# Performance work log

Measured on AMD Instinct MI355X. Metric: run time of the kernel, lower is better.

## Reference

```python
import jax, jax.numpy as jnp
import numpy as np

N_WIRES = 16
N_LAYERS = 6
BATCH = 128


def setup_inputs() -> dict:
    key = jax.random.key(0)
    k1, k2 = jax.random.split(key)
    # embedding angles in [-pi, pi]
    x = jax.random.uniform(k1, (BATCH, N_WIRES), jnp.float32, -np.pi, np.pi)
    # StronglyEntanglingLayers weights, as in __init__: 0.2 * normal
    w = 0.2 * jax.random.normal(k2, (N_LAYERS, N_WIRES, 3), jnp.float32)
    return {"x": x, "w": w}


def _apply_1q(psi, U, wire, n):
    # psi: (B, 2^n) complex; U: (2,2) or (B,2,2) complex. Wire 0 = most significant bit.
    B = psi.shape[0]
    psi = psi.reshape(B, 2 ** wire, 2, -1)
    if U.ndim == 2:
        out = jnp.einsum('ab,nlbr->nlar', U, psi)
    else:
        out = jnp.einsum('nab,nlbr->nlar', U, psi)
    return out.reshape(B, -1)


def _apply_cnot(psi, c, t, n):
    # CNOT with control c, target t: flip target axis on the control=1 subspace.
    B = psi.shape[0]
    psi = psi.reshape((B,) + (2,) * n)
    ac, at = c + 1, t + 1  # tensor axes (axis 0 is batch)
    a0 = jnp.take(psi, 0, axis=ac)
    a1 = jnp.take(psi, 1, axis=ac)
    t_ax = at - 1 if at > ac else at  # target axis after removing control axis
    a1 = jnp.flip(a1, axis=t_ax)
    psi = jnp.stack([a0, a1], axis=ac)
    return psi.reshape(B, -1)


def _rot_matrix(phi, theta, omega):
    # PennyLane Rot(phi, theta, omega) = RZ(omega) RY(theta) RZ(phi)
    c, s = jnp.cos(theta / 2), jnp.sin(theta / 2)
    m00 = jnp.exp(-0.5j * (phi + omega)) * c
    m01 = -jnp.exp(0.5j * (phi - omega)) * s
    m10 = jnp.exp(-0.5j * (phi - omega)) * s
    m11 = jnp.exp(0.5j * (phi + omega)) * c
    return jnp.stack([jnp.stack([m00, m01]), jnp.stack([m10, m11])]).astype(jnp.complex64)


def _circuit(x, w):
    B, n = x.shape
    n_layers = w.shape[0]
    psi = jnp.zeros((B, 2 ** n), jnp.complex64).at[:, 0].set(1.0)

    # AngleEmbedding, rotation='Y': RY(x_i) on wire i (batched 2x2, real entries)
    c, s = jnp.cos(x / 2), jnp.sin(x / 2)  # (B, n)
    for i in range(n):
        U = jnp.stack([jnp.stack([c[:, i], -s[:, i]], -1),
                       jnp.stack([s[:, i], c[:, i]], -1)], -2).astype(jnp.complex64)
        psi = _apply_1q(psi, U, i, n)

    # StronglyEntanglingLayers: per layer, Rot on every wire then ring of CNOTs
    for l in range(n_layers):
        for i in range(n):
            U = _rot_matrix(w[l, i, 0], w[l, i, 1], w[l, i, 2])
            psi = _apply_1q(psi, U, i, n)
        r = (l % (n - 1)) + 1 if n > 1 else 0  # default PennyLane ranges
        if r:
            for i in range(n):
                psi = _apply_cnot(psi, i, (i + r) % n, n)

    # <Z_i> = P(bit_i = 0) - P(bit_i = 1)
    probs = psi.real ** 2 + psi.imag ** 2  # (B, 2^n)
    p = probs.reshape((B,) + (2,) * n)
    z = []
    for i in range(n):
        axes = tuple(a for a in range(1, n + 1) if a != i + 1)
        m = p.sum(axis=axes)  # (B, 2)
        z.append(m[:, 0] - m[:, 1])
    return jnp.stack(z, axis=-1).astype(jnp.float32)  # (B, n_wires)


def reference(x, w):
    return _circuit(x, w)
```

## Files before the change

### kernel.cpp

```cpp
#include <hip/hip_runtime.h>
#include <utility>


#define NW    16
#define BLK   1024
#define CHUNK 16384

template<class F, int... Is>
__device__ __forceinline__ void static_for_impl(F&& f, std::integer_sequence<int, Is...>) {
    (f(std::integral_constant<int, Is>{}), ...);
}
template<int N, class F>
__device__ __forceinline__ void static_for(F&& f) {
    static_for_impl(f, std::make_integer_sequence<int, N>{});
}

__device__ __forceinline__ int swz(int u) { return u ^ (((u >> 4) & 7) << 1); }

__device__ __forceinline__ void c2x2(float2& a0, float2& a1,
                                     float2 m00, float2 m01,
                                     float2 m10, float2 m11) {
    float2 r0, r1;
    r0.x = m00.x*a0.x - m00.y*a0.y + m01.x*a1.x - m01.y*a1.y;
    r0.y = m00.x*a0.y + m00.y*a0.x + m01.x*a1.y + m01.y*a1.x;
    r1.x = m10.x*a0.x - m10.y*a0.y + m11.x*a1.x - m11.y*a1.y;
    r1.y = m10.x*a0.y + m10.y*a0.x + m11.x*a1.y + m11.y*a1.x;
    a0 = r0; a1 = r1;
}

__device__ __forceinline__ float2 cmul(float2 a, float2 b) {
    return make_float2(a.x*b.x - a.y*b.y, a.x*b.y + a.y*b.x);
}

template<int Q>
__device__ __forceinline__ void rot_regs(float2 a[16], float2 m00, float2 m01,
                                         float2 m10, float2 m11) {
#pragma unroll
    for (int j = 0; j < 16; ++j)
        if (!((j >> Q) & 1))
            c2x2(a[j], a[j | (1 << Q)], m00, m01, m10, m11);
}

template<int QC, int QT>
__device__ __forceinline__ void cnot_inreg(float2 a[16]) {
#pragma unroll
    for (int j = 0; j < 16; ++j)
        if (((j >> QC) & 1) && !((j >> QT) & 1)) {
            float2 t = a[j]; a[j] = a[j | (1 << QT)]; a[j | (1 << QT)] = t;
        }
}

template<int QT>
__device__ __forceinline__ void cnot_ctrlout(float2 a[16], int ctrl) {
#pragma unroll
    for (int j = 0; j < 16; ++j)
        if (!((j >> QT) & 1)) {
            int j2 = j | (1 << QT);
            float2 x = a[j], y = a[j2];
            a[j].x  = ctrl ? y.x : x.x;  a[j].y  = ctrl ? y.y : x.y;
            a[j2].x = ctrl ? x.x : y.x;  a[j2].y = ctrl ? x.y : y.y;
        }
}

__device__ __forceinline__ void rot_mat(const float* ww, float2 m[4]) {
    float phi = ww[0], th = ww[1], om = ww[2];
    float ct, st;   sincosf(0.5f * th, &st, &ct);
    float cap, sap; sincosf(0.5f * (phi + om), &sap, &cap);
    float cam, sam; sincosf(0.5f * (phi - om), &sam, &cam);
    m[0] = make_float2( cap * ct, -sap * ct);
    m[1] = make_float2(-cam * st, -sam * st);
    m[2] = make_float2( cam * st, -sam * st);
    m[3] = make_float2( cap * ct,  sap * ct);
}

template<int L, int S>
__device__ __forceinline__ int sweep_gates(float2 a[16], const float2 (*gm)[4],
                                           int ub, int c14) {
    constexpr int r    = L + 1;
    constexpr int base = (S == 1) ? 10 : (S == 2) ? 6 : (S == 3) ? 2 : 0;
    constexpr int plo  = base;
    constexpr int phi  = (S == 4) ? 1 : base + 3;
    int wmask = 0;
    static_for<phi - plo + 1>([&](auto K) {
        constexpr int bb = phi - decltype(K)::value;
        if constexpr (bb != 15 - r && !(L == 0 && bb == 14 - r)) {
            constexpr int wire = 15 - bb;
            rot_regs<bb - base>(a, gm[wire][0], gm[wire][1], gm[wire][2], gm[wire][3]);
        }
    });
    if constexpr (L >= 1 && (14 - r) >= plo && (14 - r) <= phi)
        cnot_ctrlout<14 - r - base>(a, c14);
    static_for<14 - r>([&](auto K) {
        constexpr int i  = 2 + decltype(K)::value;
        constexpr int cb = 15 - i, tb = cb - r;
        if constexpr (tb >= plo && tb <= phi) {
            if constexpr (cb <= base + 3) {
                cnot_inreg<cb - base, tb - base>(a);
            } else if constexpr (tb - r >= plo) {
                cnot_ctrlout<tb - base>(a, (ub >> cb) & 1);
            } else {
                wmask |= ((ub >> cb) & 1) << (tb - base);
            }
        }
    });
    return wmask;
}

template<int L>
__global__ __launch_bounds__(BLK)
void k_p1(const float* __restrict__ w, float2* __restrict__ psi) {
    constexpr int r  = L + 1;
    constexpr int G1 = 14 - L;
    const int b = blockIdx.x >> 2, m = blockIdx.x & 3;
    const int T = (m << 10) | (int)threadIdx.x;
    float2* g = psi + ((size_t)b << 16);

    const int sb = ((T & ((1 << (13 - L)) - 1)) << 1) | ((T >> (13 - L)) << (15 - L));

    float2 m0[4], m1[4], mr[4];
    rot_mat(w + (L * NW + 0) * 3, m0);
    rot_mat(w + (L * NW + 1) * 3, m1);
    rot_mat(w + (L * NW + r) * 3, mr);

    float2 a[16];
#pragma unroll
    for (int jh = 0; jh < 8; ++jh) {
        int s = sb | ((jh & 1) << G1) | (((jh >> 1) & 1) << 14) | (((jh >> 2) & 1) << 15);
        float4 f = *reinterpret_cast<const float4*>(g + s);
        a[(jh << 1)]     = make_float2(f.x, f.y);
        a[(jh << 1) | 1] = make_float2(f.z, f.w);
    }

    if constexpr (L == 1) {
        cnot_inreg<0, 3>(a);
    } else if constexpr (L == 2) {
        cnot_ctrlout<3>(a, (sb >> 1) & 1);
        cnot_inreg<0, 2>(a);
    } else {
        cnot_ctrlout<3>(a, (sb >> (L - 1)) & 1);
        cnot_ctrlout<2>(a, (sb >> (L - 2)) & 1);
    }
    rot_regs<3>(a, m0[0], m0[1], m0[2], m0[3]);
    rot_regs<2>(a, m1[0], m1[1], m1[2], m1[3]);
    rot_regs<1>(a, mr[0], mr[1], mr[2], mr[3]);
    cnot_inreg<3, 1>(a);

#pragma unroll
    for (int jh = 0; jh < 8; ++jh) {
        int s = sb | ((jh & 1) << G1) | (((jh >> 1) & 1) << 14) | (((jh >> 2) & 1) << 15);
        float2 lo = a[(jh << 1)], hi = a[(jh << 1) | 1];
        *reinterpret_cast<float4*>(g + s) = make_float4(lo.x, lo.y, hi.x, hi.y);
    }
}

template<int L>
__global__ __launch_bounds__(BLK)
void k_p2(const float* __restrict__ x, const float* __restrict__ w,
          float* __restrict__ out, float2* __restrict__ psi) {
    constexpr int r = L + 1;
    __shared__ float2 lds[CHUNK];
    __shared__ float2 gm[NW][4];
    __shared__ float  ecs[NW], ess[NW], accs[NW];
    const int b = blockIdx.x >> 2, c = blockIdx.x & 3;
    const int tid = threadIdx.x;
    const int c14 = c & 1;
    float2* g = psi + ((size_t)b << 16) + ((size_t)c << 14);

    if (tid < NW) {
        rot_mat(w + (L * NW + tid) * 3, gm[tid]);
        if (L == 0) {
            float s_, c_; sincosf(0.5f * x[b * NW + tid], &s_, &c_);
            ecs[tid] = c_; ess[tid] = s_;
        }
        if (L == 5) accs[tid] = 0.f;
    }

    if constexpr (L >= 1) {
#pragma unroll
        for (int it = 0; it < 8; ++it) {
            int v = tid + it * BLK;
            float4 f = reinterpret_cast<const float4*>(g)[v];
            int u = swz(2 * v);
            lds[u]     = make_float2(f.x, f.y);
            lds[u ^ 1] = make_float2(f.z, f.w);
        }
    }
    __syncthreads();

    float2 a[16];
    {
        const int ub = tid;
        if constexpr (L == 0) {
            float2 v[3][2];
#pragma unroll
            for (int wq = 0; wq < 3; ++wq)
#pragma unroll
                for (int bb = 0; bb < 2; ++bb) {
                    v[wq][bb].x = gm[wq][2*bb].x * ecs[wq] + gm[wq][2*bb+1].x * ess[wq];
                    v[wq][bb].y = gm[wq][2*bb].y * ecs[wq] + gm[wq][2*bb+1].y * ess[wq];
                }
            const int b0 = (c >> 1) & 1, b1 = c & 1;
            float2 psiC[2];
#pragma unroll
            for (int b2 = 0; b2 < 2; ++b2)
                psiC[b2] = cmul(cmul(v[0][b0], v[1][b1 ^ b0]), v[2][b2 ^ b1]);
            float plo = 1.0f;
#pragma unroll
            for (int k = 0; k < 10; ++k)
                plo *= ((tid >> k) & 1) ? ess[15 - k] : ecs[15 - k];
#pragma unroll
            for (int j = 0; j < 16; ++j) {
                float f3 = ((j >> 2) & 1) ? ess[3] : ecs[3];
                float f4 = ((j >> 1) & 1) ? ess[4] : ecs[4];
                float f5 = (j & 1)        ? ess[5] : ecs[5];
                float hb = f3 * f4 * f5 * plo;
                float2 pc = psiC[(j >> 3) & 1];
                a[j] = make_float2(pc.x * hb, pc.y * hb);
            }
        } else {
#pragma unroll
            for (int j = 0; j < 16; ++j) a[j] = lds[swz(ub | (j << 10))];
        }
        int wm = sweep_gates<L, 1>(a, gm, ub, c14) << 10;
#pragma unroll
        for (int j = 0; j < 16; ++j) lds[swz((ub | (j << 10)) ^ wm)] = a[j];
    }
    __syncthreads();
    {
        const int ub = (tid & 63) | ((tid >> 6) << 10);
#pragma unroll
        for (int j = 0; j < 16; ++j) a[j] = lds[swz(ub | (j << 6))];
        int wm = sweep_gates<L, 2>(a, gm, ub, c14) << 6;
#pragma unroll
        for (int j = 0; j < 16; ++j) lds[swz((ub | (j << 6)) ^ wm)] = a[j];
    }
    __syncthreads();
    {
        const int ub = (tid & 3) | ((tid >> 2) << 6);
#pragma unroll
        for (int j = 0; j < 16; ++j) a[j] = lds[swz(ub | (j << 2))];
        int wm = sweep_gates<L, 3>(a, gm, ub, c14) << 2;
#pragma unroll
        for (int j = 0; j < 16; ++j) lds[swz((ub | (j << 2)) ^ wm)] = a[j];
    }
    __syncthreads();
    {
        const int ub = tid << 4;
#pragma unroll
        for (int j = 0; j < 16; ++j) a[j] = lds[swz(ub | j)];
        int wm = sweep_gates<L, 4>(a, gm, ub, c14);
#pragma unroll
        for (int j = 0; j < 16; ++j) lds[swz((ub | j) ^ wm)] = a[j];
    }
    __syncthreads();

    if constexpr (L == 5) {
        const int ub = tid;
        float psum = 0.f, z2s = 0.f, z3s = 0.f, z4s = 0.f, z5s = 0.f;
#pragma unroll
        for (int j = 0; j < 16; ++j) {
            float2 v2 = lds[swz(ub | (j << 10))];
            float p = v2.x * v2.x + v2.y * v2.y;
            psum += p;
            z2s += (j & 8) ? -p : p;
            z3s += (j & 4) ? -p : p;
            z4s += (j & 2) ? -p : p;
            z5s += (j & 1) ? -p : p;
        }
        float z[NW];
        z[0] = (((c >> 1) ^ (tid >> 5)) & 1) ? -psum : psum;
        z[1] = (((c) ^ (tid >> 4)) & 1) ? -psum : psum;
        z[2] = ((tid >> 3) & 1) ? -z2s : z2s;
        z[3] = ((tid >> 2) & 1) ? -z3s : z3s;
        z[4] = ((tid >> 1) & 1) ? -z4s : z4s;
        z[5] = (tid & 1) ? -z5s : z5s;
#pragma unroll
        for (int i = 6; i < NW; ++i)
            z[i] = ((tid >> (15 - i)) & 1) ? -psum : psum;
#pragma unroll
        for (int i = 0; i < NW; ++i) {
            float v2 = z[i];
#pragma unroll
            for (int off = 32; off > 0; off >>= 1) v2 += __shfl_down(v2, off, 64);
            if ((tid & 63) == 0) atomicAdd(&accs[i], v2);
        }
        __syncthreads();
        if (tid < NW) atomicAdd(&out[b * NW + tid], accs[tid]);
    } else {
#pragma unroll
        for (int it = 0; it < 8; ++it) {
            int v = tid + it * BLK;
            int u = 2 * v;
            int wm0 = 0, wm1 = 0;
            static_for<(r >= 3) ? (r - 2) : 0>([&](auto K) {
                constexpr int k  = decltype(K)::value;
                constexpr int cb = r - 3 - k, tb = 13 - k;
                wm0 |= ((u >> cb) & 1) << tb;
                wm1 |= (((u | 1) >> cb) & 1) << tb;
            });
            float2 lo = lds[swz(u ^ wm0)];
            float2 hi = lds[swz((u | 1) ^ wm1)];
            reinterpret_cast<float4*>(g)[v] = make_float4(lo.x, lo.y, hi.x, hi.y);
        }
    }
}

extern "C" void kernel_launch(void* const* d_in, const int* in_sizes, int n_in,
                              void* d_out, int out_size, void* d_ws, size_t ws_size,
                              hipStream_t stream) {
    const float* x = (const float*)d_in[0];
    const float* w = (const float*)d_in[1];
    float* out = (float*)d_out;
    float2* psi = (float2*)d_ws;

    const int batch = in_sizes[0] / NW;
    const int grid  = batch * 4;

    hipMemsetAsync(d_out, 0, (size_t)out_size * sizeof(float), stream);

    k_p2<0><<<grid, BLK, 0, stream>>>(x, w, out, psi);
    k_p1<1><<<grid, BLK, 0, stream>>>(w, psi);
    k_p2<1><<<grid, BLK, 0, stream>>>(x, w, out, psi);
    k_p1<2><<<grid, BLK, 0, stream>>>(w, psi);
    k_p2<2><<<grid, BLK, 0, stream>>>(x, w, out, psi);
    k_p1<3><<<grid, BLK, 0, stream>>>(w, psi);
    k_p2<3><<<grid, BLK, 0, stream>>>(x, w, out, psi);
    k_p1<4><<<grid, BLK, 0, stream>>>(w, psi);
    k_p2<4><<<grid, BLK, 0, stream>>>(x, w, out, psi);
    k_p1<5><<<grid, BLK, 0, stream>>>(w, psi);
    k_p2<5><<<grid, BLK, 0, stream>>>(x, w, out, psi);
}
```

Baseline: 573.1 us.

## Split state into 8 chunks per sample with padded LDS and fused gather

Each phase-2 kernel now handles 8K-amplitude chunks with 512 threads instead of 16K with 1024, and repartitions which wires live in the per-block chunk versus the phase-1 kernel. The XOR swizzle is replaced by padding every 16 elements to avoid LDS bank conflicts. The first sweep now loads straight from global memory, skipping the separate LDS staging pass, and the final expectation reduction works from registers without writing back to LDS. The intent is to raise occupancy (launch_bounds 512,4) and cut LDS traffic. The cost is extra gate bookkeeping in phase 1 and more blocks, with a risk of uncoalesced global reads in the first sweep.

```diff
diff --git a/kernel.cpp b/kernel.cpp
--- a/kernel.cpp
+++ b/kernel.cpp
@@ -3,8 +3,10 @@
 
 
 #define NW    16
-#define BLK   1024
-#define CHUNK 16384
+#define P1BLK 1024
+#define P2BLK 512
+#define CHUNK 8192
+#define LDSN  (CHUNK + CHUNK / 16)
 
 template<class F, int... Is>
 __device__ __forceinline__ void static_for_impl(F&& f, std::integer_sequence<int, Is...>) {
@@ -15,7 +17,7 @@
     static_for_impl(f, std::make_integer_sequence<int, N>{});
 }
 
-__device__ __forceinline__ int swz(int u) { return u ^ (((u >> 4) & 7) << 1); }
+__device__ __forceinline__ int pidx(int u) { return u + (u >> 4); }
 
 __device__ __forceinline__ void c2x2(float2& a0, float2& a1,
                                      float2 m00, float2 m01,
@@ -73,98 +75,108 @@
     m[3] = make_float2( cap * ct,  sap * ct);
 }
 
+constexpr int swof(int tb) { return tb >= 9 ? 1 : tb >= 5 ? 2 : tb >= 1 ? 3 : 4; }
+
 template<int L, int S>
 __device__ __forceinline__ int sweep_gates(float2 a[16], const float2 (*gm)[4],
-                                           int ub, int c14) {
+                                           int ub, int c) {
     constexpr int r    = L + 1;
-    constexpr int base = (S == 1) ? 10 : (S == 2) ? 6 : (S == 3) ? 2 : 0;
-    constexpr int plo  = base;
-    constexpr int phi  = (S == 4) ? 1 : base + 3;
+    constexpr int base = (S == 1) ? 9 : (S == 2) ? 5 : (S == 3) ? 1 : 0;
+    constexpr int rlo  = base;
+    constexpr int rhi  = (S == 1) ? 12 : (S == 2) ? 8 : (S == 3) ? 4 : 0;
+    static_for<rhi - rlo + 1>([&](auto K) {
+        constexpr int bb   = rhi - decltype(K)::value;
+        constexpr int wire = 15 - bb;
+        rot_regs<bb - base>(a, gm[wire][0], gm[wire][1], gm[wire][2], gm[wire][3]);
+    });
     int wmask = 0;
-    static_for<phi - plo + 1>([&](auto K) {
-        constexpr int bb = phi - decltype(K)::value;
-        if constexpr (bb != 15 - r && !(L == 0 && bb == 14 - r)) {
-            constexpr int wire = 15 - bb;
-            rot_regs<bb - base>(a, gm[wire][0], gm[wire][1], gm[wire][2], gm[wire][3]);
-        }
-    });
-    if constexpr (L >= 1 && (14 - r) >= plo && (14 - r) <= phi)
-        cnot_ctrlout<14 - r - base>(a, c14);
-    static_for<14 - r>([&](auto K) {
-        constexpr int i  = 2 + decltype(K)::value;
-        constexpr int cb = 15 - i, tb = cb - r;
-        if constexpr (tb >= plo && tb <= phi) {
-            if constexpr (cb <= base + 3) {
-                cnot_inreg<cb - base, tb - base>(a);
-            } else if constexpr (tb - r >= plo) {
-                cnot_ctrlout<tb - base>(a, (ub >> cb) & 1);
-            } else {
-                wmask |= ((ub >> cb) & 1) << (tb - base);
+    static_for<16>([&](auto I) {
+        constexpr int i = decltype(I)::value;
+        if constexpr (i + r < 16) {
+            constexpr int cb = 15 - i, tb = cb - r;
+            constexpr bool skip = (L == 0 && i <= 1) || (L == 1 && i == 0);
+            if constexpr (!skip && swof(tb) == S) {
+                if constexpr (cb >= base && cb <= base + 3) {
+                    cnot_inreg<cb - base, tb - base>(a);
+                } else {
+                    int ctrl = (cb >= 13) ? ((c >> (cb - 13)) & 1)
+                                          : ((ub >> cb) & 1);
+                    constexpr int ts = tb - r;
+                    if constexpr (ts >= 0 && swof(ts) == S)
+                        cnot_ctrlout<tb - base>(a, ctrl);
+                    else
+                        wmask |= ctrl << (tb - base);
+                }
             }
         }
     });
     return wmask;
 }
 
-template<int L>
-__global__ __launch_bounds__(BLK)
+template<int LL>
+__global__ __launch_bounds__(P1BLK)
 void k_p1(const float* __restrict__ w, float2* __restrict__ psi) {
-    constexpr int r  = L + 1;
-    constexpr int G1 = 14 - L;
-    const int b = blockIdx.x >> 2, m = blockIdx.x & 3;
-    const int T = (m << 10) | (int)threadIdx.x;
+    const int b = blockIdx.x >> 2;
+    const int T = ((blockIdx.x & 3) << 10) | (int)threadIdx.x;
     float2* g = psi + ((size_t)b << 16);
-
-    const int sb = ((T & ((1 << (13 - L)) - 1)) << 1) | ((T >> (13 - L)) << (15 - L));
-
-    float2 m0[4], m1[4], mr[4];
-    rot_mat(w + (L * NW + 0) * 3, m0);
-    rot_mat(w + (L * NW + 1) * 3, m1);
-    rot_mat(w + (L * NW + r) * 3, mr);
+    const int sb = T << 1;
+
+    float2 m0[4], m1[4], m2[4];
+    rot_mat(w + (LL * NW + 0) * 3, m0);
+    rot_mat(w + (LL * NW + 1) * 3, m1);
+    rot_mat(w + (LL * NW + 2) * 3, m2);
 
     float2 a[16];
 #pragma unroll
     for (int jh = 0; jh < 8; ++jh) {
-        int s = sb | ((jh & 1) << G1) | (((jh >> 1) & 1) << 14) | (((jh >> 2) & 1) << 15);
+        int s = sb | ((jh & 1) << 13) | (((jh >> 1) & 1) << 14) | (((jh >> 2) & 1) << 15);
         float4 f = *reinterpret_cast<const float4*>(g + s);
         a[(jh << 1)]     = make_float2(f.x, f.y);
         a[(jh << 1) | 1] = make_float2(f.z, f.w);
     }
 
-    if constexpr (L == 1) {
+    if constexpr (LL == 1) {
         cnot_inreg<0, 3>(a);
-    } else if constexpr (L == 2) {
+    } else if constexpr (LL == 2) {
         cnot_ctrlout<3>(a, (sb >> 1) & 1);
         cnot_inreg<0, 2>(a);
+    } else if constexpr (LL == 3) {
+        cnot_ctrlout<3>(a, (sb >> 2) & 1);
+        cnot_ctrlout<2>(a, (sb >> 1) & 1);
+        cnot_inreg<0, 1>(a);
+    } else if constexpr (LL == 4) {
+        cnot_ctrlout<3>(a, (sb >> 3) & 1);
+        cnot_ctrlout<2>(a, (sb >> 2) & 1);
+        cnot_ctrlout<1>(a, (sb >> 1) & 1);
     } else {
-        cnot_ctrlout<3>(a, (sb >> (L - 1)) & 1);
-        cnot_ctrlout<2>(a, (sb >> (L - 2)) & 1);
-    }
+        cnot_ctrlout<3>(a, (sb >> 4) & 1);
+        cnot_ctrlout<2>(a, (sb >> 3) & 1);
+        cnot_ctrlout<1>(a, (sb >> 2) & 1);
+    }
+
     rot_regs<3>(a, m0[0], m0[1], m0[2], m0[3]);
     rot_regs<2>(a, m1[0], m1[1], m1[2], m1[3]);
-    rot_regs<1>(a, mr[0], mr[1], mr[2], mr[3]);
-    cnot_inreg<3, 1>(a);
+    rot_regs<1>(a, m2[0], m2[1], m2[2], m2[3]);
+    if constexpr (LL == 1) cnot_inreg<3, 1>(a);
 
 #pragma unroll
     for (int jh = 0; jh < 8; ++jh) {
-        int s = sb | ((jh & 1) << G1) | (((jh >> 1) & 1) << 14) | (((jh >> 2) & 1) << 15);
+        int s = sb | ((jh & 1) << 13) | (((jh >> 1) & 1) << 14) | (((jh >> 2) & 1) << 15);
         float2 lo = a[(jh << 1)], hi = a[(jh << 1) | 1];
         *reinterpret_cast<float4*>(g + s) = make_float4(lo.x, lo.y, hi.x, hi.y);
     }
 }
 
 template<int L>
-__global__ __launch_bounds__(BLK)
+__global__ __launch_bounds__(P2BLK, 4)
 void k_p2(const float* __restrict__ x, const float* __restrict__ w,
           float* __restrict__ out, float2* __restrict__ psi) {
-    constexpr int r = L + 1;
-    __shared__ float2 lds[CHUNK];
+    __shared__ float2 lds[LDSN];
     __shared__ float2 gm[NW][4];
     __shared__ float  ecs[NW], ess[NW], accs[NW];
-    const int b = blockIdx.x >> 2, c = blockIdx.x & 3;
+    const int b = blockIdx.x >> 3, c = blockIdx.x & 7;
     const int tid = threadIdx.x;
-    const int c14 = c & 1;
-    float2* g = psi + ((size_t)b << 16) + ((size_t)c << 14);
+    float2* g = psi + ((size_t)b << 16) + ((size_t)c << 13);
 
     if (tid < NW) {
         rot_mat(w + (L * NW + tid) * 3, gm[tid]);
@@ -174,17 +186,6 @@
         }
         if (L == 5) accs[tid] = 0.f;
     }
-
-    if constexpr (L >= 1) {
-#pragma unroll
-        for (int it = 0; it < 8; ++it) {
-            int v = tid + it * BLK;
-            float4 f = reinterpret_cast<const float4*>(g)[v];
-            int u = swz(2 * v);
-            lds[u]     = make_float2(f.x, f.y);
-            lds[u ^ 1] = make_float2(f.z, f.w);
-        }
-    }
     __syncthreads();
 
     float2 a[16];
@@ -199,108 +200,108 @@
                     v[wq][bb].x = gm[wq][2*bb].x * ecs[wq] + gm[wq][2*bb+1].x * ess[wq];
                     v[wq][bb].y = gm[wq][2*bb].y * ecs[wq] + gm[wq][2*bb+1].y * ess[wq];
                 }
-            const int b0 = (c >> 1) & 1, b1 = c & 1;
-            float2 psiC[2];
-#pragma unroll
-            for (int b2 = 0; b2 < 2; ++b2)
-                psiC[b2] = cmul(cmul(v[0][b0], v[1][b1 ^ b0]), v[2][b2 ^ b1]);
+            const int c2 = (c >> 2) & 1, c1 = (c >> 1) & 1, c0 = c & 1;
+            float2 cs = cmul(cmul(v[0][c2], v[1][c1 ^ c2]), v[2][c0 ^ c1]);
             float plo = 1.0f;
 #pragma unroll
-            for (int k = 0; k < 10; ++k)
+            for (int k = 0; k < 9; ++k)
                 plo *= ((tid >> k) & 1) ? ess[15 - k] : ecs[15 - k];
 #pragma unroll
             for (int j = 0; j < 16; ++j) {
-                float f3 = ((j >> 2) & 1) ? ess[3] : ecs[3];
-                float f4 = ((j >> 1) & 1) ? ess[4] : ecs[4];
-                float f5 = (j & 1)        ? ess[5] : ecs[5];
-                float hb = f3 * f4 * f5 * plo;
-                float2 pc = psiC[(j >> 3) & 1];
-                a[j] = make_float2(pc.x * hb, pc.y * hb);
+                float f = plo * ((j & 8) ? ess[3] : ecs[3])
+                              * ((j & 4) ? ess[4] : ecs[4])
+                              * ((j & 2) ? ess[5] : ecs[5])
+                              * ((j & 1) ? ess[6] : ecs[6]);
+                a[j] = make_float2(cs.x * f, cs.y * f);
             }
         } else {
 #pragma unroll
-            for (int j = 0; j < 16; ++j) a[j] = lds[swz(ub | (j << 10))];
-        }
-        int wm = sweep_gates<L, 1>(a, gm, ub, c14) << 10;
-#pragma unroll
-        for (int j = 0; j < 16; ++j) lds[swz((ub | (j << 10)) ^ wm)] = a[j];
+            for (int j = 0; j < 16; ++j)
+                a[j] = g[tid | (j << 9)];
+        }
+        int wm = sweep_gates<L, 1>(a, gm, ub, c) << 9;
+#pragma unroll
+        for (int j = 0; j < 16; ++j) lds[pidx((tid | (j << 9)) ^ wm)] = a[j];
     }
     __syncthreads();
     {
-        const int ub = (tid & 63) | ((tid >> 6) << 10);
-#pragma unroll
-        for (int j = 0; j < 16; ++j) a[j] = lds[swz(ub | (j << 6))];
-        int wm = sweep_gates<L, 2>(a, gm, ub, c14) << 6;
-#pragma unroll
-        for (int j = 0; j < 16; ++j) lds[swz((ub | (j << 6)) ^ wm)] = a[j];
+        const int ub = (tid & 31) | ((tid >> 5) << 9);
+#pragma unroll
+        for (int j = 0; j < 16; ++j) a[j] = lds[pidx(ub | (j << 5))];
+        int wm = sweep_gates<L, 2>(a, gm, ub, c) << 5;
+#pragma unroll
+        for (int j = 0; j < 16; ++j) lds[pidx((ub | (j << 5)) ^ wm)] = a[j];
     }
     __syncthreads();
     {
-        const int ub = (tid & 3) | ((tid >> 2) << 6);
-#pragma unroll
-        for (int j = 0; j < 16; ++j) a[j] = lds[swz(ub | (j << 2))];
-        int wm = sweep_gates<L, 3>(a, gm, ub, c14) << 2;
-#pragma unroll
-        for (int j = 0; j < 16; ++j) lds[swz((ub | (j << 2)) ^ wm)] = a[j];
+        const int ub = (tid & 1) | ((tid >> 1) << 5);
+#pragma unroll
+        for (int j = 0; j < 16; ++j) a[j] = lds[pidx(ub | (j << 1))];
+        int wm = sweep_gates<L, 3>(a, gm, ub, c) << 1;
+#pragma unroll
+        for (int j = 0; j < 16; ++j) lds[pidx((ub | (j << 1)) ^ wm)] = a[j];
     }
     __syncthreads();
     {
         const int ub = tid << 4;
 #pragma unroll
-        for (int j = 0; j < 16; ++j) a[j] = lds[swz(ub | j)];
-        int wm = sweep_gates<L, 4>(a, gm, ub, c14);
-#pragma unroll
-        for (int j = 0; j < 16; ++j) lds[swz((ub | j) ^ wm)] = a[j];
-    }
-    __syncthreads();
-
-    if constexpr (L == 5) {
-        const int ub = tid;
-        float psum = 0.f, z2s = 0.f, z3s = 0.f, z4s = 0.f, z5s = 0.f;
-#pragma unroll
-        for (int j = 0; j < 16; ++j) {
-            float2 v2 = lds[swz(ub | (j << 10))];
-            float p = v2.x * v2.x + v2.y * v2.y;
-            psum += p;
-            z2s += (j & 8) ? -p : p;
-            z3s += (j & 4) ? -p : p;
-            z4s += (j & 2) ? -p : p;
-            z5s += (j & 1) ? -p : p;
-        }
-        float z[NW];
-        z[0] = (((c >> 1) ^ (tid >> 5)) & 1) ? -psum : psum;
-        z[1] = (((c) ^ (tid >> 4)) & 1) ? -psum : psum;
-        z[2] = ((tid >> 3) & 1) ? -z2s : z2s;
-        z[3] = ((tid >> 2) & 1) ? -z3s : z3s;
-        z[4] = ((tid >> 1) & 1) ? -z4s : z4s;
-        z[5] = (tid & 1) ? -z5s : z5s;
-#pragma unroll
-        for (int i = 6; i < NW; ++i)
-            z[i] = ((tid >> (15 - i)) & 1) ? -psum : psum;
-#pragma unroll
-        for (int i = 0; i < NW; ++i) {
-            float v2 = z[i];
-#pragma unroll
-            for (int off = 32; off > 0; off >>= 1) v2 += __shfl_down(v2, off, 64);
-            if ((tid & 63) == 0) atomicAdd(&accs[i], v2);
-        }
-        __syncthreads();
-        if (tid < NW) atomicAdd(&out[b * NW + tid], accs[tid]);
-    } else {
-#pragma unroll
-        for (int it = 0; it < 8; ++it) {
-            int v = tid + it * BLK;
-            int u = 2 * v;
-            int wm0 = 0, wm1 = 0;
-            static_for<(r >= 3) ? (r - 2) : 0>([&](auto K) {
-                constexpr int k  = decltype(K)::value;
-                constexpr int cb = r - 3 - k, tb = 13 - k;
-                wm0 |= ((u >> cb) & 1) << tb;
-                wm1 |= (((u | 1) >> cb) & 1) << tb;
-            });
-            float2 lo = lds[swz(u ^ wm0)];
-            float2 hi = lds[swz((u | 1) ^ wm1)];
-            reinterpret_cast<float4*>(g)[v] = make_float4(lo.x, lo.y, hi.x, hi.y);
+        for (int j = 0; j < 16; ++j) a[j] = lds[pidx(ub | j)];
+        int wm = sweep_gates<L, 4>(a, gm, ub, c);
+
+        if constexpr (L == 5) {
+            float psum = 0.f, sb3 = 0.f, sb2 = 0.f, sb1 = 0.f, sb0 = 0.f;
+#pragma unroll
+            for (int j = 0; j < 16; ++j) {
+                int jj = j ^ wm;
+                float2 v2 = a[j];
+                float p = v2.x * v2.x + v2.y * v2.y;
+                psum += p;
+                sb3 += (jj & 8) ? -p : p;
+                sb2 += (jj & 4) ? -p : p;
+                sb1 += (jj & 2) ? -p : p;
+                sb0 += (jj & 1) ? -p : p;
+            }
+            const int c2 = (c >> 2) & 1, c1 = (c >> 1) & 1, c0 = c & 1;
+            float z[NW];
+            z[0]  = ((c2 ^ (tid >> 1)) & 1) ? -psum : psum;
+            z[1]  = ((c1 ^ tid) & 1)        ? -psum : psum;
+            z[2]  = c0 ? -sb3 : sb3;
+            z[3]  = ((tid >> 8) & 1) ? -sb2 : sb2;
+            z[4]  = ((tid >> 7) & 1) ? -sb1 : sb1;
+            z[5]  = ((tid >> 6) & 1) ? -sb0 : sb0;
+#pragma unroll
+            for (int i = 6; i < 12; ++i)
+                z[i] = ((tid >> (11 - i)) & 1) ? -psum : psum;
+            z[12] = sb3; z[13] = sb2; z[14] = sb1; z[15] = sb0;
+#pragma unroll
+            for (int i = 0; i < NW; ++i) {
+                float v2 = z[i];
+#pragma unroll
+                for (int off = 32; off > 0; off >>= 1)
+                    v2 += __shfl_down(v2, off, 64);
+                if ((tid & 63) == 0) atomicAdd(&accs[i], v2);
+            }
+            __syncthreads();
+            if (tid < NW) atomicAdd(&out[b * NW + tid], accs[tid]);
+        } else {
+#pragma unroll
+            for (int j = 0; j < 16; ++j) lds[pidx((ub | j) ^ wm)] = a[j];
+            __syncthreads();
+#pragma unroll
+            for (int it = 0; it < CHUNK / 2 / P2BLK; ++it) {
+                int v = tid + it * P2BLK;
+                int u = 2 * v;
+                int wm0 = 0, wm1 = 0;
+                static_for<(L >= 3) ? (L - 2) : 0>([&](auto K) {
+                    constexpr int k  = decltype(K)::value;
+                    constexpr int cbb = L - 3 - k, tbb = 12 - k;
+                    wm0 |= ((u >> cbb) & 1) << tbb;
+                    wm1 |= (((u | 1) >> cbb) & 1) << tbb;
+                });
+                float2 lo = lds[pidx(u ^ wm0)];
+                float2 hi = lds[pidx((u | 1) ^ wm1)];
+                reinterpret_cast<float4*>(g)[v] = make_float4(lo.x, lo.y, hi.x, hi.y);
+            }
         }
     }
 }
@@ -314,19 +315,20 @@
     float2* psi = (float2*)d_ws;
 
     const int batch = in_sizes[0] / NW;
-    const int grid  = batch * 4;
+    const int g1 = batch * 4;
+    const int g2 = batch * 8;
 
     hipMemsetAsync(d_out, 0, (size_t)out_size * sizeof(float), stream);
 
-    k_p2<0><<<grid, BLK, 0, stream>>>(x, w, out, psi);
-    k_p1<1><<<grid, BLK, 0, stream>>>(w, psi);
-    k_p2<1><<<grid, BLK, 0, stream>>>(x, w, out, psi);
-    k_p1<2><<<grid, BLK, 0, stream>>>(w, psi);
-    k_p2<2><<<grid, BLK, 0, stream>>>(x, w, out, psi);
-    k_p1<3><<<grid, BLK, 0, stream>>>(w, psi);
-    k_p2<3><<<grid, BLK, 0, stream>>>(x, w, out, psi);
-    k_p1<4><<<grid, BLK, 0, stream>>>(w, psi);
-    k_p2<4><<<grid, BLK, 0, stream>>>(x, w, out, psi);
-    k_p1<5><<<grid, BLK, 0, stream>>>(w, psi);
-    k_p2<5><<<grid, BLK, 0, stream>>>(x, w, out, psi);
-}
+    k_p2<0><<<g2, P2BLK, 0, stream>>>(x, w, out, psi);
+    k_p1<1><<<g1, P1BLK, 0, stream>>>(w, psi);
+    k_p2<1><<<g2, P2BLK, 0, stream>>>(x, w, out, psi);
+    k_p1<2><<<g1, P1BLK, 0, stream>>>(w, psi);
+    k_p2<2><<<g2, P2BLK, 0, stream>>>(x, w, out, psi);
+    k_p1<3><<<g1, P1BLK, 0, stream>>>(w, psi);
+    k_p2<3><<<g2, P2BLK, 0, stream>>>(x, w, out, psi);
+    k_p1<4><<<g1, P1BLK, 0, stream>>>(w, psi);
+    k_p2<4><<<g2, P2BLK, 0, stream>>>(x, w, out, psi);
+    k_p1<5><<<g1, P1BLK, 0, stream>>>(w, psi);
+    k_p2<5><<<g2, P2BLK, 0, stream>>>(x, w, out, psi);
+}
```

Measured after the change: 493.6 us. -13.9%, faster.
